# Performance work log

Measured on AMD Instinct MI355X. Metric: run time of the kernel, lower is better.

The kernel has to match this reference:

```python
import jax, jax.numpy as jnp
import numpy as np

DIM = 128
HEADS = 4
DIM_HEAD = 32
EPS = 1e-5


def layer_norm(x, w, b):
    mu = jnp.mean(x, axis=-1, keepdims=True)
    var = jnp.mean(jnp.square(x - mu), axis=-1, keepdims=True)
    return (x - mu) * jax.lax.rsqrt(var + EPS) * w + b


def setup_inputs() -> dict:
    key = jax.random.key(0)
    ks = jax.random.split(key, 16)
    B, N, D, bH, bW = 2, 6, DIM, 50, 50
    iH, iW = 24, 56
    HD = HEADS * DIM_HEAD
    w = lambda k, shp: (jax.random.normal(k, shp, jnp.float32) * 0.02)
    inp = {
        "q": jax.random.normal(ks[0], (B, N, D, bH, bW), jnp.float32),
        "k": jax.random.normal(ks[1], (B, N, D, iH, iW), jnp.float32),
        "v": jax.random.normal(ks[2], (B, N, D, iH, iW), jnp.float32),
        "skip": jax.random.normal(ks[3], (B, D, bH, bW), jnp.float32),
        "ln_q_w": jnp.ones((D,), jnp.float32), "ln_q_b": jnp.zeros((D,), jnp.float32),
        "wq": w(ks[4], (D, HD)), "bq": jnp.zeros((HD,), jnp.float32),
        "ln_k_w": jnp.ones((D,), jnp.float32), "ln_k_b": jnp.zeros((D,), jnp.float32),
        "wk": w(ks[5], (D, HD)), "bk": jnp.zeros((HD,), jnp.float32),
        "ln_v_w": jnp.ones((D,), jnp.float32), "ln_v_b": jnp.zeros((D,), jnp.float32),
        "wv": w(ks[6], (D, HD)), "bv": jnp.zeros((HD,), jnp.float32),
        "wo": w(ks[7], (HD, D)), "bo": jnp.zeros((D,), jnp.float32),
        "ln_pre_w": jnp.ones((D,), jnp.float32), "ln_pre_b": jnp.zeros((D,), jnp.float32),
        "w1": w(ks[8], (D, 2 * D)), "b1": jnp.zeros((2 * D,), jnp.float32),
        "w2": w(ks[9], (2 * D, D)), "b2": jnp.zeros((D,), jnp.float32),
        "ln_post_w": jnp.ones((D,), jnp.float32), "ln_post_b": jnp.zeros((D,), jnp.float32),
    }
    return inp


def reference(q, k, v, skip,
              ln_q_w, ln_q_b, wq, bq,
              ln_k_w, ln_k_b, wk, bk,
              ln_v_w, ln_v_b, wv, bv,
              wo, bo, ln_pre_w, ln_pre_b,
              w1, b1, w2, b2, ln_post_w, ln_post_b):
    B, N, D, bH, bW = q.shape
    iH, iW = k.shape[-2:]
    Q, K = bH * bW, iH * iW
    scale = D ** (-0.5)  # NOTE: original uses dim**-0.5, not dim_head

    # queries: (B,N,D,Q) -> (B,N,Q,D) -> LN -> linear -> (B,N,Q,H,Dh)
    qf = jnp.transpose(q.reshape(B, N, D, Q), (0, 1, 3, 2))
    qh = (layer_norm(qf, ln_q_w, ln_q_b) @ wq + bq).reshape(B, N, Q, HEADS, DIM_HEAD)
    # keys: (B,N,D,K) -> (B,N,K,D)
    kf = jnp.transpose(k.reshape(B, N, D, K), (0, 1, 3, 2))
    kh = (layer_norm(kf, ln_k_w, ln_k_b) @ wk + bk).reshape(B, N, K, HEADS, DIM_HEAD)
    # values: (B,N,D,iH,iW) -> (B,N,iH,iW,D) -> (B,N*K,D)
    vf = jnp.transpose(v, (0, 1, 3, 4, 2)).reshape(B, N * K, D)
    vh = (layer_norm(vf, ln_v_w, ln_v_b) @ wv + bv).reshape(B, N * K, HEADS, DIM_HEAD)

    # logits: (B,N,Q,K,H) -> (B,Q,N*K,H), softmax over combined N*K axis
    logits = scale * jnp.einsum('bnqmd,bnkmd->bnqkm', qh, kh)
    logits = jnp.transpose(logits, (0, 2, 1, 3, 4)).reshape(B, Q, N * K, HEADS)
    att = jax.nn.softmax(logits, axis=-2)

    a = jnp.einsum('bqkm,bkmd->bqmd', att, vh).reshape(B, Q, HEADS * DIM_HEAD)
    z = a @ wo + bo  # (B,Q,D)
    z = z + jnp.transpose(skip.reshape(B, D, Q), (0, 2, 1))
    z = layer_norm(z, ln_pre_w, ln_pre_b)
    z = z + (jax.nn.gelu(z @ w1 + b1, approximate=False) @ w2 + b2)
    z = layer_norm(z, ln_post_w, ln_post_b)
    return jnp.transpose(z.reshape(B, bH, bW, D), (0, 3, 1, 2))
```

## Files before the change

### kernel.cpp

```cpp
#include <hip/hip_runtime.h>
#include <hip/hip_bf16.h>

#define QP 2500
#define KP 1344
#define SCALE 0.088388347648318447f
#define LOG2E 1.4426950408889634f
#define LNEPS 1e-5f

typedef __attribute__((ext_vector_type(8))) short bf16x8;
typedef __attribute__((ext_vector_type(4))) float f32x4;
typedef __attribute__((ext_vector_type(16))) float f32x16;

__device__ inline ushort f2bf(float x) {
  uint u = __float_as_uint(x);
  return (ushort)((u + 0x7fffu + ((u >> 16) & 1u)) >> 16);
}

union Frag8 { uint2 u[2]; bf16x8 f; ushort us[8]; };

__device__ inline bf16x8 ldfrag_swz(const char* rowbase, int colbyte, int C) {
  Frag8 t;
  t.u[0] = *(const uint2*)(rowbase + ((colbyte) ^ C));
  t.u[1] = *(const uint2*)(rowbase + ((colbyte + 8) ^ C));
  return t.f;
}

__device__ inline uint pk2(float a, float b) {
  union { __hip_bfloat162 h; uint u; } cv;
  cv.h = __float22bfloat162_rn(make_float2(a, b));
  return cv.u;
}

__device__ inline void gld16(const ushort* g, ushort* l) {
  __builtin_amdgcn_global_load_lds(
      (const __attribute__((address_space(1))) void*)g,
      (__attribute__((address_space(3))) void*)l, 16, 0, 0);
}

__global__ __launch_bounds__(256) void wprep_kernel(
    const float* __restrict__ wq, const float* __restrict__ wk, const float* __restrict__ wv,
    ushort* __restrict__ wtq, ushort* __restrict__ wtk, ushort* __restrict__ wtv)
{
  const float* W = (blockIdx.y == 0) ? wq : (blockIdx.y == 1) ? wk : wv;
  ushort* WT = (blockIdx.y == 0) ? wtq : (blockIdx.y == 1) ? wtk : wtv;
  const int t = threadIdx.x;
  const int idx = blockIdx.x * 1024 + t * 4;
  const int k = idx >> 7, j0 = idx & 127;
  float4 rd = *(const float4*)&W[idx];
  WT[(j0 + 0) * 128 + k] = f2bf(rd.x);
  WT[(j0 + 1) * 128 + k] = f2bf(rd.y);
  WT[(j0 + 2) * 128 + k] = f2bf(rd.z);
  WT[(j0 + 3) * 128 + k] = f2bf(rd.w);
}

__global__ __launch_bounds__(256) void wprep2_kernel(
    const float* __restrict__ wo, const float* __restrict__ w1, const float* __restrict__ w2,
    ushort* __restrict__ woT, ushort* __restrict__ w1T, ushort* __restrict__ w2T)
{
  const int y = blockIdx.y;
  const float* W; ushort* WT; int jsh, K, total;
  if (y == 0)      { W = wo; WT = woT; jsh = 7; K = 128; total = 16384; }
  else if (y == 1) { W = w1; WT = w1T; jsh = 8; K = 128; total = 32768; }
  else             { W = w2; WT = w2T; jsh = 7; K = 256; total = 32768; }
  const int idx = blockIdx.x * 1024 + threadIdx.x * 4;
  if (idx >= total) return;
  const int k = idx >> jsh, j0 = idx & ((1 << jsh) - 1);
  float4 rd = *(const float4*)&W[idx];
  WT[(j0 + 0) * K + k] = f2bf(rd.x);
  WT[(j0 + 1) * K + k] = f2bf(rd.y);
  WT[(j0 + 2) * K + k] = f2bf(rd.z);
  WT[(j0 + 3) * K + k] = f2bf(rd.w);
}

__global__ __launch_bounds__(256) void proj_kernel(
    const float* __restrict__ qin, const float* __restrict__ kin, const float* __restrict__ vin,
    const float* __restrict__ lnqw, const float* __restrict__ lnqb,
    const float* __restrict__ lnkw, const float* __restrict__ lnkb,
    const float* __restrict__ lnvw, const float* __restrict__ lnvb,
    const ushort* __restrict__ wtq_, const ushort* __restrict__ wtk_, const ushort* __restrict__ wtv_,
    const float* __restrict__ bq_, const float* __restrict__ bk_, const float* __restrict__ bv_,
    ushort* __restrict__ qout, ushort* __restrict__ kout, ushort* __restrict__ vtout)
{
  const int z = blockIdx.z;
  if (z > 0 && blockIdx.x >= 21) return;

  const float *in, *lnw, *lnb, *bias;
  const ushort* WT;
  int P;
  if (z == 0)      { in = qin; lnw = lnqw; lnb = lnqb; WT = wtq_; bias = bq_; P = QP; }
  else if (z == 1) { in = kin; lnw = lnkw; lnb = lnkb; WT = wtk_; bias = bk_; P = KP; }
  else             { in = vin; lnw = lnvw; lnb = lnvb; WT = wtv_; bias = bv_; P = KP; }

  __shared__ __align__(16) ushort xb[64][128];
  __shared__ __align__(16) ushort wt[128][128];
  __shared__ float ps[4][64], pq[4][64];
  __shared__ float mu_s[64], rs_s[64];

  const int bn = blockIdx.y;
  const int p0 = blockIdx.x * 64;
  const int t  = threadIdx.x;
  const int w = t >> 6, lane = t & 63, g = lane >> 4, ln15 = lane & 15;

  #pragma unroll
  for (int i = 0; i < 8; ++i) {
    int idx8 = t + 256 * i;
    int j = idx8 >> 4, ck = (idx8 & 15) * 16;
    *(uint4*)((char*)wt + j * 256 + (ck ^ ((j & 7) << 4))) =
        *(const uint4*)((const char*)WT + j * 256 + ck);
  }

  const float* src = in + ((size_t)bn * 128) * P + p0;
  const int p = t & 63, dq = t >> 6;
  float xv[32];
  float s = 0.f, s2 = 0.f;
  #pragma unroll
  for (int kk = 0; kk < 32; ++kk) {
    int d = dq + 4 * kk;
    float v = (p0 + p < P) ? src[(size_t)d * P + p] : 0.f;
    xv[kk] = v; s += v; s2 += v * v;
  }
  ps[dq][p] = s; pq[dq][p] = s2;
  __syncthreads();
  if (t < 64) {
    float a = ps[0][t] + ps[1][t] + ps[2][t] + ps[3][t];
    float b = pq[0][t] + pq[1][t] + pq[2][t] + pq[3][t];
    float mu = a * (1.f / 128.f);
    float var = b * (1.f / 128.f) - mu * mu;
    mu_s[t] = mu; rs_s[t] = rsqrtf(var + LNEPS);
  }
  __syncthreads();
  {
    const float mu = mu_s[p], rs = rs_s[p];
    const int CW = (p & 7) << 4;
    #pragma unroll
    for (int kk = 0; kk < 32; ++kk) {
      int d = dq + 4 * kk;
      float v = (xv[kk] - mu) * rs * lnw[d] + lnb[d];
      *(ushort*)((char*)xb + p * 256 + ((2 * d) ^ CW)) = f2bf(v);
    }
  }
  __syncthreads();

  const int prow = w * 16 + ln15;
  const char* xrow = (const char*)xb + prow * 256;
  const int CX = (prow & 7) << 4;
  const int CB = (ln15 & 7) << 4;
  const f32x4 zf = {0.f, 0.f, 0.f, 0.f};
  f32x4 acc[8];
  #pragma unroll
  for (int jc = 0; jc < 8; ++jc) acc[jc] = zf;

  #pragma unroll
  for (int ks = 0; ks < 4; ++ks) {
    bf16x8 a = ldfrag_swz(xrow, ks * 64 + g * 16, CX);
    #pragma unroll
    for (int jc = 0; jc < 8; ++jc) {
      bf16x8 b = ldfrag_swz((const char*)wt + (jc * 16 + ln15) * 256, ks * 64 + g * 16, CB);
      acc[jc] = __builtin_amdgcn_mfma_f32_16x16x32_bf16(a, b, acc[jc], 0, 0, 0);
    }
  }

  if (z == 0) {
    const float os = SCALE * LOG2E;
    #pragma unroll
    for (int jc = 0; jc < 8; ++jc) {
      const float bj = bias[jc * 16 + ln15];
      #pragma unroll
      for (int r = 0; r < 4; ++r) {
        int pr = p0 + w * 16 + 4 * g + r;
        if (pr < P)
          qout[((size_t)bn * P + pr) * 128 + jc * 16 + ln15] = f2bf((acc[jc][r] + bj) * os);
      }
    }
  } else if (z == 1) {
    #pragma unroll
    for (int jc = 0; jc < 8; ++jc) {
      const int j = jc * 16 + ln15;
      const int h = j >> 5, dh32 = j & 31;
      const int c = dh32 >> 3, e = dh32 & 7;
      const float bj = bias[j];
      #pragma unroll
      for (int r4 = 0; r4 < 4; ++r4) {
        int pp = p0 + w * 16 + 4 * g + r4;
        int kt = pp >> 6, r = pp & 63;
        int l2 = r >> 1;
        int pz = ((r & 1) * 4 + c + l2) & 7;
        kout[(size_t)((bn * 4 + h) * 21 + kt) * 2048 + l2 * 64 + pz * 8 + e] =
            f2bf(acc[jc][r4] + bj);
      }
    }
  } else {
    #pragma unroll
    for (int jc = 0; jc < 8; ++jc) {
      const int j = jc * 16 + ln15;
      const int h = j >> 5, rdh = j & 31;
      const float bj = bias[j];
      #pragma unroll
      for (int r4 = 0; r4 < 4; ++r4) {
        int pp = p0 + w * 16 + 4 * g + r4;
        int kt = pp >> 6, kk = pp & 63;
        int ch = (kk >> 3) ^ (rdh & 7);
        vtout[(size_t)((bn * 4 + h) * 21 + kt) * 2048 + rdh * 64 + ch * 8 + (kk & 7)] =
            f2bf(acc[jc][r4] + bj);
      }
    }
  }
}

__global__ __launch_bounds__(128, 4) void attn_kernel(
    const ushort* __restrict__ qh, const ushort* __restrict__ kimg,
    const ushort* __restrict__ vimg, float* __restrict__ aw,
    float* __restrict__ ml)
{
  __shared__ __align__(16) ushort Kb[2][2048];
  __shared__ __align__(16) ushort Vb[2][2048];

  const int lin = blockIdx.x + 40 * (blockIdx.y + 4 * blockIdx.z);
  const int sid = (lin & 7) * 240 + (lin >> 3);
  const int bx = sid % 40;
  const int hh = (sid / 40) & 3;
  const int bn = sid / 160;

  const int q0 = bx * 64;
  const int t = threadIdx.x;
  const int w = t >> 6;
  const int lane = t & 63;
  const int lk = lane & 31;
  const int hi = lane >> 5;

  bf16x8 qf0, qf1;
  {
    Frag8 z_; z_.u[0] = make_uint2(0, 0); z_.u[1] = make_uint2(0, 0);
    int qrow = q0 + w * 32 + lk;
    if (qrow < QP) {
      const ushort* qp = &qh[((size_t)bn * QP + qrow) * 128 + hh * 32 + hi * 8];
      qf0 = *(const bf16x8*)(qp);
      qf1 = *(const bf16x8*)(qp + 16);
    } else { qf0 = z_.f; qf1 = z_.f; }
  }

  const ushort* ksrc = kimg + (size_t)((bn * 4 + hh) * 21) * 2048 + w * 1024 + lane * 8;
  const ushort* vsrc = vimg + (size_t)((bn * 4 + hh) * 21) * 2048 + w * 1024 + lane * 8;

  gld16(ksrc,       &Kb[0][w * 1024]);
  gld16(ksrc + 512, &Kb[0][w * 1024 + 512]);
  gld16(vsrc,       &Vb[0][w * 1024]);
  gld16(vsrc + 512, &Vb[0][w * 1024 + 512]);
  __syncthreads();

  f32x16 O;
  #pragma unroll
  for (int i = 0; i < 16; ++i) O[i] = 0.f;
  float lpart = 0.f;

  for (int kt = 0; kt < 21; ++kt) {
    const int cur = kt & 1;
    if (kt < 20) {
      const ushort* kp = ksrc + (size_t)(kt + 1) * 2048;
      const ushort* vp = vsrc + (size_t)(kt + 1) * 2048;
      gld16(kp,       &Kb[cur ^ 1][w * 1024]);
      gld16(kp + 512, &Kb[cur ^ 1][w * 1024 + 512]);
      gld16(vp,       &Vb[cur ^ 1][w * 1024]);
      gld16(vp + 512, &Vb[cur ^ 1][w * 1024 + 512]);
    }
    const char* Kbase = (const char*)Kb[cur];
    const char* Vbase = (const char*)Vb[cur];

    #pragma unroll
    for (int kc2 = 0; kc2 < 2; ++kc2) {
      f32x16 S;
      #pragma unroll
      for (int i = 0; i < 16; ++i) S[i] = 0.f;
      {
        const int l2 = kc2 * 16 + (lk >> 1);
        const int pb = (lk & 1) * 4 + hi + l2;
        bf16x8 kfa = *(const bf16x8*)(Kbase + l2 * 128 + ((pb + 0) & 7) * 16);
        bf16x8 kfb = *(const bf16x8*)(Kbase + l2 * 128 + ((pb + 2) & 7) * 16);
        S = __builtin_amdgcn_mfma_f32_32x32x16_bf16(kfa, qf0, S, 0, 0, 0);
        S = __builtin_amdgcn_mfma_f32_32x32x16_bf16(kfb, qf1, S, 0, 0, 0);
      }

      float e0 = exp2f(S[0]),  e1 = exp2f(S[1]),  e2 = exp2f(S[2]),  e3 = exp2f(S[3]);
      float e4 = exp2f(S[4]),  e5 = exp2f(S[5]),  e6 = exp2f(S[6]),  e7 = exp2f(S[7]);
      float e8 = exp2f(S[8]),  e9 = exp2f(S[9]),  e10 = exp2f(S[10]), e11 = exp2f(S[11]);
      float e12 = exp2f(S[12]), e13 = exp2f(S[13]), e14 = exp2f(S[14]), e15 = exp2f(S[15]);
      lpart += (((e0 + e1) + (e2 + e3)) + ((e4 + e5) + (e6 + e7)))
             + (((e8 + e9) + (e10 + e11)) + ((e12 + e13) + (e14 + e15)));
      uint w0 = pk2(e0, e1),  w1 = pk2(e2, e3),  w2 = pk2(e4, e5),  w3 = pk2(e6, e7);
      uint w4 = pk2(e8, e9),  w5 = pk2(e10, e11), w6 = pk2(e12, e13), w7 = pk2(e14, e15);

      asm volatile("v_permlane32_swap_b32 %0, %1" : "+v"(w2), "+v"(w0));
      asm volatile("v_permlane32_swap_b32 %0, %1" : "+v"(w3), "+v"(w1));
      asm volatile("v_permlane32_swap_b32 %0, %1" : "+v"(w6), "+v"(w4));
      asm volatile("v_permlane32_swap_b32 %0, %1" : "+v"(w7), "+v"(w5));

      Frag8 pa0, pa1;
      pa0.u[0] = make_uint2(w0, w1); pa0.u[1] = make_uint2(w2, w3);
      pa1.u[0] = make_uint2(w4, w5); pa1.u[1] = make_uint2(w6, w7);
      bf16x8 vf0 = *(const bf16x8*)(Vbase + lk * 128 + (((kc2 * 4 + 0 + hi) ^ (lk & 7)) * 16));
      bf16x8 vf1 = *(const bf16x8*)(Vbase + lk * 128 + (((kc2 * 4 + 2 + hi) ^ (lk & 7)) * 16));
      O = __builtin_amdgcn_mfma_f32_32x32x16_bf16(pa0.f, vf0, O, 0, 0, 0);
      O = __builtin_amdgcn_mfma_f32_32x32x16_bf16(pa1.f, vf1, O, 0, 0, 0);
    }
    __syncthreads();
  }

  float lsum = lpart + __shfl_xor(lpart, 32);
  {
    int qrow = q0 + w * 32 + lk;
    if (hi == 0 && qrow < QP)
      ml[((size_t)bn * QP + qrow) * 4 + hh] = lsum;
  }
  #pragma unroll
  for (int reg = 0; reg < 16; ++reg) {
    int crow = (reg & 3) + 8 * (reg >> 2) + 4 * hi;
    int qrow = q0 + w * 32 + crow;
    if (qrow < QP)
      aw[((size_t)bn * QP + qrow) * 128 + hh * 32 + lk] = O[reg];
  }
}

__global__ __launch_bounds__(256) void epilogue_kernel(
    const float* __restrict__ aw, const float* __restrict__ ml,
    const float* __restrict__ skip,
    const ushort* __restrict__ woT, const float* __restrict__ bo,
    const float* __restrict__ lnpw, const float* __restrict__ lnpb,
    const ushort* __restrict__ w1T, const float* __restrict__ b1,
    const ushort* __restrict__ w2T, const float* __restrict__ b2,
    const float* __restrict__ lnqw, const float* __restrict__ lnqb,
    float* __restrict__ out)
{
  __shared__ __align__(16) ushort xa[16][128];
  __shared__ __align__(16) ushort znb[16][128];
  __shared__ __align__(16) ushort hb[16][256];
  __shared__ float skp[128][17];
  __shared__ float2 red[4][16];
  __shared__ float mu_s[16], rs_s[16];
  __shared__ float cc[16][4];

  const int b = blockIdx.y;
  const int q0 = blockIdx.x * 16;
  const int t = threadIdx.x;
  const int w = t >> 6, lane = t & 63, g = lane >> 4, ln15 = lane & 15;
  const f32x4 zf = {0.f, 0.f, 0.f, 0.f};

  if (t < 64) {
    int r = t >> 2, h = t & 3;
    int qrow = q0 + r;
    float inv = 0.f;
    if (qrow < QP) {
      float sum = 0.f;
      #pragma unroll
      for (int n = 0; n < 6; ++n)
        sum += ml[((size_t)(b * 6 + n) * QP + qrow) * 4 + h];
      inv = 1.f / sum;
    }
    cc[r][h] = inv;
  }
  #pragma unroll
  for (int i = 0; i < 8; ++i) {
    int idx = t + 256 * i;
    int j = idx >> 4, r = idx & 15;
    int qrow = q0 + r;
    skp[j][r] = (qrow < QP) ? skip[((size_t)b * 128 + j) * QP + qrow] : 0.f;
  }
  __syncthreads();

  #pragma unroll
  for (int i = 0; i < 4; ++i) {
    int idx = t + 256 * i;
    int r = idx >> 6, jp = idx & 63;
    int qrow = q0 + r;
    float v0 = 0.f, v1 = 0.f;
    if (qrow < QP) {
      #pragma unroll
      for (int n = 0; n < 6; ++n) {
        float2 p = *(const float2*)&aw[((size_t)(b * 6 + n) * QP + qrow) * 128 + 2 * jp];
        v0 += p.x; v1 += p.y;
      }
      float iv = cc[r][jp >> 4];
      v0 *= iv; v1 *= iv;
    }
    *(uint*)((char*)xa + r * 256 + ((4 * jp) ^ ((r & 7) << 4))) = pk2(v0, v1);
  }
  __syncthreads();

  f32x4 acc1[2] = {zf, zf};
  #pragma unroll
  for (int ks = 0; ks < 4; ++ks) {
    bf16x8 a = ldfrag_swz((const char*)xa + ln15 * 256, ks * 64 + g * 16, (ln15 & 7) << 4);
    #pragma unroll
    for (int jc = 0; jc < 2; ++jc) {
      int j = (2 * w + jc) * 16 + ln15;
      bf16x8 bfr = *(const bf16x8*)&woT[j * 128 + ks * 32 + g * 8];
      acc1[jc] = __builtin_amdgcn_mfma_f32_16x16x32_bf16(a, bfr, acc1[jc], 0, 0, 0);
    }
  }
  float z[2][4];
  #pragma unroll
  for (int jc = 0; jc < 2; ++jc) {
    int j = (2 * w + jc) * 16 + ln15;
    float bj = bo[j];
    #pragma unroll
    for (int i = 0; i < 4; ++i)
      z[jc][i] = acc1[jc][i] + bj + skp[j][4 * g + i];
  }
  {
    float s_[4], q_[4];
    #pragma unroll
    for (int i = 0; i < 4; ++i) {
      s_[i] = z[0][i] + z[1][i];
      q_[i] = z[0][i] * z[0][i] + z[1][i] * z[1][i];
    }
    #pragma unroll
    for (int m = 1; m <= 8; m <<= 1) {
      #pragma unroll
      for (int i = 0; i < 4; ++i) {
        s_[i] += __shfl_xor(s_[i], m);
        q_[i] += __shfl_xor(q_[i], m);
      }
    }
    if (ln15 == 0) {
      #pragma unroll
      for (int i = 0; i < 4; ++i) red[w][4 * g + i] = make_float2(s_[i], q_[i]);
    }
  }
  __syncthreads();
  if (t < 16) {
    float S = red[0][t].x + red[1][t].x + red[2][t].x + red[3][t].x;
    float Q = red[0][t].y + red[1][t].y + red[2][t].y + red[3][t].y;
    float mu = S * (1.f / 128.f);
    float var = Q * (1.f / 128.f) - mu * mu;
    mu_s[t] = mu; rs_s[t] = rsqrtf(var + LNEPS);
  }
  __syncthreads();
  float zn[2][4];
  #pragma unroll
  for (int jc = 0; jc < 2; ++jc) {
    int j = (2 * w + jc) * 16 + ln15;
    float lw = lnpw[j], lb = lnpb[j];
    #pragma unroll
    for (int i = 0; i < 4; ++i) {
      int r = 4 * g + i;
      float v = (z[jc][i] - mu_s[r]) * rs_s[r] * lw + lb;
      zn[jc][i] = v;
      *(ushort*)((char*)znb + r * 256 + ((2 * j) ^ ((r & 7) << 4))) = f2bf(v);
    }
  }
  __syncthreads();

  f32x4 acc2[4] = {zf, zf, zf, zf};
  #pragma unroll
  for (int ks = 0; ks < 4; ++ks) {
    bf16x8 a = ldfrag_swz((const char*)znb + ln15 * 256, ks * 64 + g * 16, (ln15 & 7) << 4);
    #pragma unroll
    for (int jc2 = 0; jc2 < 4; ++jc2) {
      int j2 = (4 * w + jc2) * 16 + ln15;
      bf16x8 bfr = *(const bf16x8*)&w1T[j2 * 128 + ks * 32 + g * 8];
      acc2[jc2] = __builtin_amdgcn_mfma_f32_16x16x32_bf16(a, bfr, acc2[jc2], 0, 0, 0);
    }
  }
  #pragma unroll
  for (int jc2 = 0; jc2 < 4; ++jc2) {
    int j2 = (4 * w + jc2) * 16 + ln15;
    float bj = b1[j2];
    #pragma unroll
    for (int i = 0; i < 4; ++i) {
      float x = acc2[jc2][i] + bj;
      float ge = 0.5f * x * (1.f + erff(x * 0.70710678118654752f));
      int r = 4 * g + i;
      *(ushort*)((char*)hb + r * 512 + ((2 * j2) ^ ((r & 7) << 4))) = f2bf(ge);
    }
  }
  __syncthreads();

  f32x4 acc3[2] = {zf, zf};
  #pragma unroll
  for (int ks = 0; ks < 8; ++ks) {
    bf16x8 a = ldfrag_swz((const char*)hb + ln15 * 512, ks * 64 + g * 16, (ln15 & 7) << 4);
    #pragma unroll
    for (int jc = 0; jc < 2; ++jc) {
      int j = (2 * w + jc) * 16 + ln15;
      bf16x8 bfr = *(const bf16x8*)&w2T[j * 256 + ks * 32 + g * 8];
      acc3[jc] = __builtin_amdgcn_mfma_f32_16x16x32_bf16(a, bfr, acc3[jc], 0, 0, 0);
    }
  }
  float z2[2][4];
  #pragma unroll
  for (int jc = 0; jc < 2; ++jc) {
    int j = (2 * w + jc) * 16 + ln15;
    float bj = b2[j];
    #pragma unroll
    for (int i = 0; i < 4; ++i)
      z2[jc][i] = acc3[jc][i] + bj + zn[jc][i];
  }
  {
    float s_[4], q_[4];
    #pragma unroll
    for (int i = 0; i < 4; ++i) {
      s_[i] = z2[0][i] + z2[1][i];
      q_[i] = z2[0][i] * z2[0][i] + z2[1][i] * z2[1][i];
    }
    #pragma unroll
    for (int m = 1; m <= 8; m <<= 1) {
      #pragma unroll
      for (int i = 0; i < 4; ++i) {
        s_[i] += __shfl_xor(s_[i], m);
        q_[i] += __shfl_xor(q_[i], m);
      }
    }
    if (ln15 == 0) {
      #pragma unroll
      for (int i = 0; i < 4; ++i) red[w][4 * g + i] = make_float2(s_[i], q_[i]);
    }
  }
  __syncthreads();
  if (t < 16) {
    float S = red[0][t].x + red[1][t].x + red[2][t].x + red[3][t].x;
    float Q = red[0][t].y + red[1][t].y + red[2][t].y + red[3][t].y;
    float mu = S * (1.f / 128.f);
    float var = Q * (1.f / 128.f) - mu * mu;
    mu_s[t] = mu; rs_s[t] = rsqrtf(var + LNEPS);
  }
  __syncthreads();
  #pragma unroll
  for (int jc = 0; jc < 2; ++jc) {
    int j = (2 * w + jc) * 16 + ln15;
    float lw = lnqw[j], lb = lnqb[j];
    #pragma unroll
    for (int i = 0; i < 4; ++i) {
      int r = 4 * g + i;
      skp[j][r] = (z2[jc][i] - mu_s[r]) * rs_s[r] * lw + lb;
    }
  }
  __syncthreads();
  #pragma unroll
  for (int i = 0; i < 8; ++i) {
    int idx = t + 256 * i;
    int j = idx >> 4, r = idx & 15;
    int qrow = q0 + r;
    if (qrow < QP)
      out[((size_t)b * 128 + j) * QP + qrow] = skp[j][r];
  }
}

extern "C" void kernel_launch(void* const* d_in, const int* in_sizes, int n_in,
                              void* d_out, int out_size, void* d_ws, size_t ws_size,
                              hipStream_t stream) {
  const float* q       = (const float*)d_in[0];
  const float* k       = (const float*)d_in[1];
  const float* v       = (const float*)d_in[2];
  const float* skip    = (const float*)d_in[3];
  const float* ln_q_w  = (const float*)d_in[4];
  const float* ln_q_b  = (const float*)d_in[5];
  const float* wq      = (const float*)d_in[6];
  const float* bq      = (const float*)d_in[7];
  const float* ln_k_w  = (const float*)d_in[8];
  const float* ln_k_b  = (const float*)d_in[9];
  const float* wk      = (const float*)d_in[10];
  const float* bk      = (const float*)d_in[11];
  const float* ln_v_w  = (const float*)d_in[12];
  const float* ln_v_b  = (const float*)d_in[13];
  const float* wv      = (const float*)d_in[14];
  const float* bv      = (const float*)d_in[15];
  const float* wo      = (const float*)d_in[16];
  const float* bo      = (const float*)d_in[17];
  const float* ln_pre_w  = (const float*)d_in[18];
  const float* ln_pre_b  = (const float*)d_in[19];
  const float* w1      = (const float*)d_in[20];
  const float* b1      = (const float*)d_in[21];
  const float* w2      = (const float*)d_in[22];
  const float* b2      = (const float*)d_in[23];
  const float* ln_post_w = (const float*)d_in[24];
  const float* ln_post_b = (const float*)d_in[25];

  float* out = (float*)d_out;
  ushort* qhp  = (ushort*)d_ws;
  ushort* kimg = qhp + 3840000;
  ushort* vimg = kimg + 2064384;
  ushort* wtq  = vimg + 2064384;
  ushort* wtk  = wtq + 16384;
  ushort* wtv  = wtk + 16384;
  ushort* woT  = wtv + 16384;
  ushort* w1T  = woT + 16384;
  ushort* w2T  = w1T + 32768;
  float*  aw   = (float*)(w2T + 32768);
  float*  ml   = aw + 3840000;

  wprep_kernel<<<dim3(16, 3), 256, 0, stream>>>(wq, wk, wv, wtq, wtk, wtv);
  wprep2_kernel<<<dim3(32, 3), 256, 0, stream>>>(wo, w1, w2, woT, w1T, w2T);
  proj_kernel<<<dim3(40, 12, 3), 256, 0, stream>>>(q, k, v,
      ln_q_w, ln_q_b, ln_k_w, ln_k_b, ln_v_w, ln_v_b,
      wtq, wtk, wtv, bq, bk, bv, qhp, kimg, vimg);
  attn_kernel<<<dim3(40, 4, 12), 128, 0, stream>>>(qhp, kimg, vimg, aw, ml);
  epilogue_kernel<<<dim3(157, 2), 256, 0, stream>>>(aw, ml, skip, woT, bo,
      ln_pre_w, ln_pre_b, w1T, b1, w2T, b2, ln_post_w, ln_post_b, out);
}
```

Measured before the change: 126.5 us.

## Triple-buffer K/V tiles in attention with vmcnt-based waits and new K swizzle

The attention kernel moves from double to triple buffering of K and V tiles in LDS, prefetching two tiles ahead. It replaces __syncthreads with explicit s_waitcnt vmcnt(4) plus s_barrier, so only the older tile's loads must land before each barrier. The K image layout written by the projection kernel changes from a paired-row 8-chunk swizzle to a per-key-row 4-chunk rotation, with matching reads in attention. This hides more global-load latency at the cost of more LDS per block, which may reduce occupancy.

Result: slower. 136.2 us (+7.7%).

```diff
diff --git a/kernel.cpp b/kernel.cpp
--- a/kernel.cpp
+++ b/kernel.cpp
@@ -176,16 +176,14 @@
     #pragma unroll
     for (int jc = 0; jc < 8; ++jc) {
       const int j = jc * 16 + ln15;
-      const int h = j >> 5, dh32 = j & 31;
-      const int c = dh32 >> 3, e = dh32 & 7;
+      const int h = j >> 5, dh = j & 31, gk = dh >> 3, pos = dh & 7;
       const float bj = bias[j];
       #pragma unroll
       for (int r4 = 0; r4 < 4; ++r4) {
         int pp = p0 + w * 16 + 4 * g + r4;
         int kt = pp >> 6, r = pp & 63;
-        int l2 = r >> 1;
-        int pz = ((r & 1) * 4 + c + l2) & 7;
-        kout[(size_t)((bn * 4 + h) * 21 + kt) * 2048 + l2 * 64 + pz * 8 + e] =
+        int ch = (gk + (r >> 1)) & 3;
+        kout[(size_t)((bn * 4 + h) * 21 + kt) * 2048 + r * 32 + ch * 8 + pos] =
             f2bf(acc[jc][r4] + bj);
       }
     }
@@ -212,8 +210,8 @@
     const ushort* __restrict__ vimg, float* __restrict__ aw,
     float* __restrict__ ml)
 {
-  __shared__ __align__(16) ushort Kb[2][2048];
-  __shared__ __align__(16) ushort Vb[2][2048];
+  __shared__ __align__(16) ushort Kb[3][2048];
+  __shared__ __align__(16) ushort Vb[3][2048];
 
   const int lin = blockIdx.x + 40 * (blockIdx.y + 4 * blockIdx.z);
   const int sid = (lin & 7) * 240 + (lin >> 3);
@@ -242,40 +240,44 @@
   const ushort* ksrc = kimg + (size_t)((bn * 4 + hh) * 21) * 2048 + w * 1024 + lane * 8;
   const ushort* vsrc = vimg + (size_t)((bn * 4 + hh) * 21) * 2048 + w * 1024 + lane * 8;
 
-  gld16(ksrc,       &Kb[0][w * 1024]);
-  gld16(ksrc + 512, &Kb[0][w * 1024 + 512]);
-  gld16(vsrc,       &Vb[0][w * 1024]);
-  gld16(vsrc + 512, &Vb[0][w * 1024 + 512]);
-  __syncthreads();
+  gld16(ksrc,        &Kb[0][w * 1024]);
+  gld16(ksrc + 512,  &Kb[0][w * 1024 + 512]);
+  gld16(vsrc,        &Vb[0][w * 1024]);
+  gld16(vsrc + 512,  &Vb[0][w * 1024 + 512]);
+  gld16(ksrc + 2048, &Kb[1][w * 1024]);
+  gld16(ksrc + 2560, &Kb[1][w * 1024 + 512]);
+  gld16(vsrc + 2048, &Vb[1][w * 1024]);
+  gld16(vsrc + 2560, &Vb[1][w * 1024 + 512]);
+  asm volatile("s_waitcnt vmcnt(4)" ::: "memory");
+  __builtin_amdgcn_s_barrier();
 
   f32x16 O;
   #pragma unroll
   for (int i = 0; i < 16; ++i) O[i] = 0.f;
   float lpart = 0.f;
 
+  int cur = 0, nxt2 = 2;
   for (int kt = 0; kt < 21; ++kt) {
-    const int cur = kt & 1;
-    if (kt < 20) {
-      const ushort* kp = ksrc + (size_t)(kt + 1) * 2048;
-      const ushort* vp = vsrc + (size_t)(kt + 1) * 2048;
-      gld16(kp,       &Kb[cur ^ 1][w * 1024]);
-      gld16(kp + 512, &Kb[cur ^ 1][w * 1024 + 512]);
-      gld16(vp,       &Vb[cur ^ 1][w * 1024]);
-      gld16(vp + 512, &Vb[cur ^ 1][w * 1024 + 512]);
+    if (kt < 19) {
+      const ushort* kp = ksrc + (size_t)(kt + 2) * 2048;
+      const ushort* vp = vsrc + (size_t)(kt + 2) * 2048;
+      gld16(kp,       &Kb[nxt2][w * 1024]);
+      gld16(kp + 512, &Kb[nxt2][w * 1024 + 512]);
+      gld16(vp,       &Vb[nxt2][w * 1024]);
+      gld16(vp + 512, &Vb[nxt2][w * 1024 + 512]);
     }
     const char* Kbase = (const char*)Kb[cur];
     const char* Vbase = (const char*)Vb[cur];
 
     #pragma unroll
     for (int kc2 = 0; kc2 < 2; ++kc2) {
+      const int key = kc2 * 32 + lk;
       f32x16 S;
       #pragma unroll
       for (int i = 0; i < 16; ++i) S[i] = 0.f;
       {
-        const int l2 = kc2 * 16 + (lk >> 1);
-        const int pb = (lk & 1) * 4 + hi + l2;
-        bf16x8 kfa = *(const bf16x8*)(Kbase + l2 * 128 + ((pb + 0) & 7) * 16);
-        bf16x8 kfb = *(const bf16x8*)(Kbase + l2 * 128 + ((pb + 2) & 7) * 16);
+        bf16x8 kfa = *(const bf16x8*)(Kbase + key * 64 + (((hi     + (key >> 1)) & 3) * 16));
+        bf16x8 kfb = *(const bf16x8*)(Kbase + key * 64 + (((2 + hi + (key >> 1)) & 3) * 16));
         S = __builtin_amdgcn_mfma_f32_32x32x16_bf16(kfa, qf0, S, 0, 0, 0);
         S = __builtin_amdgcn_mfma_f32_32x32x16_bf16(kfb, qf1, S, 0, 0, 0);
       }
@@ -302,7 +304,16 @@
       O = __builtin_amdgcn_mfma_f32_32x32x16_bf16(pa0.f, vf0, O, 0, 0, 0);
       O = __builtin_amdgcn_mfma_f32_32x32x16_bf16(pa1.f, vf1, O, 0, 0, 0);
     }
-    __syncthreads();
+
+    if (kt < 19) {
+      asm volatile("s_waitcnt vmcnt(4)" ::: "memory");
+    } else if (kt == 19) {
+      asm volatile("s_waitcnt vmcnt(0)" ::: "memory");
+    }
+    __builtin_amdgcn_s_barrier();
+
+    cur = (cur == 2) ? 0 : cur + 1;
+    nxt2 = (nxt2 == 2) ? 0 : nxt2 + 1;
   }
 
   float lsum = lpart + __shfl_xor(lpart, 32);
```

## Read K/V fragments directly from global memory in attention, merge weight-prep kernels

Applied to the files above, without the earlier changes.

The attention kernel drops its LDS double-buffered K/V staging and per-tile barriers. Each wave now loads its MFMA fragments straight from global memory, relying on L2/L1 caching, and the K image layout is changed to a 32-element row swizzle to match. Blocks grow to 256 threads covering 128 queries, so more waves share cached K/V tiles, and s_setprio is wrapped around the MFMA issue. The two weight-prep launches are merged into one, saving a launch at the cost of more uncoalesced global fragment loads in the inner loop.

Result: faster. 114.6 us (-9.4%).

```diff
diff --git a/kernel.cpp b/kernel.cpp
--- a/kernel.cpp
+++ b/kernel.cpp
@@ -31,37 +31,22 @@
   return cv.u;
 }
 
-__device__ inline void gld16(const ushort* g, ushort* l) {
-  __builtin_amdgcn_global_load_lds(
-      (const __attribute__((address_space(1))) void*)g,
-      (__attribute__((address_space(3))) void*)l, 16, 0, 0);
-}
-
 __global__ __launch_bounds__(256) void wprep_kernel(
     const float* __restrict__ wq, const float* __restrict__ wk, const float* __restrict__ wv,
-    ushort* __restrict__ wtq, ushort* __restrict__ wtk, ushort* __restrict__ wtv)
-{
-  const float* W = (blockIdx.y == 0) ? wq : (blockIdx.y == 1) ? wk : wv;
-  ushort* WT = (blockIdx.y == 0) ? wtq : (blockIdx.y == 1) ? wtk : wtv;
-  const int t = threadIdx.x;
-  const int idx = blockIdx.x * 1024 + t * 4;
-  const int k = idx >> 7, j0 = idx & 127;
-  float4 rd = *(const float4*)&W[idx];
-  WT[(j0 + 0) * 128 + k] = f2bf(rd.x);
-  WT[(j0 + 1) * 128 + k] = f2bf(rd.y);
-  WT[(j0 + 2) * 128 + k] = f2bf(rd.z);
-  WT[(j0 + 3) * 128 + k] = f2bf(rd.w);
-}
-
-__global__ __launch_bounds__(256) void wprep2_kernel(
     const float* __restrict__ wo, const float* __restrict__ w1, const float* __restrict__ w2,
+    ushort* __restrict__ wtq, ushort* __restrict__ wtk, ushort* __restrict__ wtv,
     ushort* __restrict__ woT, ushort* __restrict__ w1T, ushort* __restrict__ w2T)
 {
   const int y = blockIdx.y;
   const float* W; ushort* WT; int jsh, K, total;
-  if (y == 0)      { W = wo; WT = woT; jsh = 7; K = 128; total = 16384; }
-  else if (y == 1) { W = w1; WT = w1T; jsh = 8; K = 128; total = 32768; }
-  else             { W = w2; WT = w2T; jsh = 7; K = 256; total = 32768; }
+  switch (y) {
+    case 0: W = wq; WT = wtq; jsh = 7; K = 128; total = 16384; break;
+    case 1: W = wk; WT = wtk; jsh = 7; K = 128; total = 16384; break;
+    case 2: W = wv; WT = wtv; jsh = 7; K = 128; total = 16384; break;
+    case 3: W = wo; WT = woT; jsh = 7; K = 128; total = 16384; break;
+    case 4: W = w1; WT = w1T; jsh = 8; K = 128; total = 32768; break;
+    default: W = w2; WT = w2T; jsh = 7; K = 256; total = 32768; break;
+  }
   const int idx = blockIdx.x * 1024 + threadIdx.x * 4;
   if (idx >= total) return;
   const int k = idx >> jsh, j0 = idx & ((1 << jsh) - 1);
@@ -176,16 +161,14 @@
     #pragma unroll
     for (int jc = 0; jc < 8; ++jc) {
       const int j = jc * 16 + ln15;
-      const int h = j >> 5, dh32 = j & 31;
-      const int c = dh32 >> 3, e = dh32 & 7;
+      const int h = j >> 5, dh = j & 31, gk = dh >> 3, pos = dh & 7;
       const float bj = bias[j];
       #pragma unroll
       for (int r4 = 0; r4 < 4; ++r4) {
         int pp = p0 + w * 16 + 4 * g + r4;
         int kt = pp >> 6, r = pp & 63;
-        int l2 = r >> 1;
-        int pz = ((r & 1) * 4 + c + l2) & 7;
-        kout[(size_t)((bn * 4 + h) * 21 + kt) * 2048 + l2 * 64 + pz * 8 + e] =
+        int ch = (gk + (r >> 1)) & 3;
+        kout[(size_t)((bn * 4 + h) * 21 + kt) * 2048 + r * 32 + ch * 8 + pos] =
             f2bf(acc[jc][r4] + bj);
       }
     }
@@ -207,21 +190,18 @@
   }
 }
 
-__global__ __launch_bounds__(128, 4) void attn_kernel(
+__global__ __launch_bounds__(256, 4) void attn_kernel(
     const ushort* __restrict__ qh, const ushort* __restrict__ kimg,
     const ushort* __restrict__ vimg, float* __restrict__ aw,
     float* __restrict__ ml)
 {
-  __shared__ __align__(16) ushort Kb[2][2048];
-  __shared__ __align__(16) ushort Vb[2][2048];
-
-  const int lin = blockIdx.x + 40 * (blockIdx.y + 4 * blockIdx.z);
-  const int sid = (lin & 7) * 240 + (lin >> 3);
-  const int bx = sid % 40;
-  const int hh = (sid / 40) & 3;
-  const int bn = sid / 160;
-
-  const int q0 = bx * 64;
+  const int lin = blockIdx.x + 20 * (blockIdx.y + 4 * blockIdx.z);
+  const int sid = (lin & 7) * 120 + (lin >> 3);
+  const int bx = sid % 20;
+  const int hh = (sid / 20) & 3;
+  const int bn = sid / 80;
+
+  const int q0 = bx * 128;
   const int t = threadIdx.x;
   const int w = t >> 6;
   const int lane = t & 63;
@@ -239,14 +219,9 @@
     } else { qf0 = z_.f; qf1 = z_.f; }
   }
 
-  const ushort* ksrc = kimg + (size_t)((bn * 4 + hh) * 21) * 2048 + w * 1024 + lane * 8;
-  const ushort* vsrc = vimg + (size_t)((bn * 4 + hh) * 21) * 2048 + w * 1024 + lane * 8;
-
-  gld16(ksrc,       &Kb[0][w * 1024]);
-  gld16(ksrc + 512, &Kb[0][w * 1024 + 512]);
-  gld16(vsrc,       &Vb[0][w * 1024]);
-  gld16(vsrc + 512, &Vb[0][w * 1024 + 512]);
-  __syncthreads();
+  const size_t slab = (size_t)((bn * 4 + hh) * 21) * 2048;
+  const ushort* kb = kimg + slab;
+  const ushort* vb = vimg + slab;
 
   f32x16 O;
   #pragma unroll
@@ -254,30 +229,22 @@
   float lpart = 0.f;
 
   for (int kt = 0; kt < 21; ++kt) {
-    const int cur = kt & 1;
-    if (kt < 20) {
-      const ushort* kp = ksrc + (size_t)(kt + 1) * 2048;
-      const ushort* vp = vsrc + (size_t)(kt + 1) * 2048;
-      gld16(kp,       &Kb[cur ^ 1][w * 1024]);
-      gld16(kp + 512, &Kb[cur ^ 1][w * 1024 + 512]);
-      gld16(vp,       &Vb[cur ^ 1][w * 1024]);
-      gld16(vp + 512, &Vb[cur ^ 1][w * 1024 + 512]);
-    }
-    const char* Kbase = (const char*)Kb[cur];
-    const char* Vbase = (const char*)Vb[cur];
+    const ushort* kp = kb + (size_t)kt * 2048;
+    const ushort* vp = vb + (size_t)kt * 2048;
 
     #pragma unroll
     for (int kc2 = 0; kc2 < 2; ++kc2) {
+      const int key = kc2 * 32 + lk;
       f32x16 S;
       #pragma unroll
       for (int i = 0; i < 16; ++i) S[i] = 0.f;
       {
-        const int l2 = kc2 * 16 + (lk >> 1);
-        const int pb = (lk & 1) * 4 + hi + l2;
-        bf16x8 kfa = *(const bf16x8*)(Kbase + l2 * 128 + ((pb + 0) & 7) * 16);
-        bf16x8 kfb = *(const bf16x8*)(Kbase + l2 * 128 + ((pb + 2) & 7) * 16);
+        bf16x8 kfa = *(const bf16x8*)(kp + key * 32 + ((hi     + (key >> 1)) & 3) * 8);
+        bf16x8 kfb = *(const bf16x8*)(kp + key * 32 + ((2 + hi + (key >> 1)) & 3) * 8);
+        __builtin_amdgcn_s_setprio(1);
         S = __builtin_amdgcn_mfma_f32_32x32x16_bf16(kfa, qf0, S, 0, 0, 0);
         S = __builtin_amdgcn_mfma_f32_32x32x16_bf16(kfb, qf1, S, 0, 0, 0);
+        __builtin_amdgcn_s_setprio(0);
       }
 
       float e0 = exp2f(S[0]),  e1 = exp2f(S[1]),  e2 = exp2f(S[2]),  e3 = exp2f(S[3]);
@@ -297,12 +264,13 @@
       Frag8 pa0, pa1;
       pa0.u[0] = make_uint2(w0, w1); pa0.u[1] = make_uint2(w2, w3);
       pa1.u[0] = make_uint2(w4, w5); pa1.u[1] = make_uint2(w6, w7);
-      bf16x8 vf0 = *(const bf16x8*)(Vbase + lk * 128 + (((kc2 * 4 + 0 + hi) ^ (lk & 7)) * 16));
-      bf16x8 vf1 = *(const bf16x8*)(Vbase + lk * 128 + (((kc2 * 4 + 2 + hi) ^ (lk & 7)) * 16));
+      bf16x8 vf0 = *(const bf16x8*)(vp + lk * 64 + (((kc2 * 4 + 0 + hi) ^ (lk & 7)) * 8));
+      bf16x8 vf1 = *(const bf16x8*)(vp + lk * 64 + (((kc2 * 4 + 2 + hi) ^ (lk & 7)) * 8));
+      __builtin_amdgcn_s_setprio(1);
       O = __builtin_amdgcn_mfma_f32_32x32x16_bf16(pa0.f, vf0, O, 0, 0, 0);
       O = __builtin_amdgcn_mfma_f32_32x32x16_bf16(pa1.f, vf1, O, 0, 0, 0);
-    }
-    __syncthreads();
+      __builtin_amdgcn_s_setprio(0);
+    }
   }
 
   float lsum = lpart + __shfl_xor(lpart, 32);
@@ -587,12 +555,12 @@
   float*  aw   = (float*)(w2T + 32768);
   float*  ml   = aw + 3840000;
 
-  wprep_kernel<<<dim3(16, 3), 256, 0, stream>>>(wq, wk, wv, wtq, wtk, wtv);
-  wprep2_kernel<<<dim3(32, 3), 256, 0, stream>>>(wo, w1, w2, woT, w1T, w2T);
+  wprep_kernel<<<dim3(32, 6), 256, 0, stream>>>(wq, wk, wv, wo, w1, w2,
+      wtq, wtk, wtv, woT, w1T, w2T);
   proj_kernel<<<dim3(40, 12, 3), 256, 0, stream>>>(q, k, v,
       ln_q_w, ln_q_b, ln_k_w, ln_k_b, ln_v_w, ln_v_b,
       wtq, wtk, wtv, bq, bk, bv, qhp, kimg, vimg);
-  attn_kernel<<<dim3(40, 4, 12), 128, 0, stream>>>(qhp, kimg, vimg, aw, ml);
+  attn_kernel<<<dim3(20, 4, 12), 256, 0, stream>>>(qhp, kimg, vimg, aw, ml);
   epilogue_kernel<<<dim3(157, 2), 256, 0, stream>>>(aw, ml, skip, woT, bo,
       ln_pre_w, ln_pre_b, w1T, b1, w2T, b2, ln_post_w, ln_post_b, out);
 }
```
